# Optimization experiments

Hardware: AMD Instinct MI355X
Metric: run time of the kernel (lower is better)

Reference implementation:

```python
import jax, jax.numpy as jnp
import numpy as np

T, B, C, H, W = 4, 8, 256, 16, 16
HEADS = 8
N = H * W
TN = T * N
DH = C // HEADS
DECAY = 0.25

# STE quantizer: fwd round(clamp(x,0,1)); bwd passes grad only where 0<=x<=1
@jax.custom_vjp
def quant1(x):
    return jnp.round(jnp.clip(x, 0.0, 1.0))

def _q_fwd(x):
    return quant1(x), x

def _q_bwd(x, g):
    return (jnp.where((x < 0) | (x > 1), 0.0, g),)

quant1.defvjp(_q_fwd, _q_bwd)

def lif(x):
    # x: [T, ...]; sequential LIF membrane decay + quantize over leading (time) axis
    def step(carry, xt):
        mem_old, spike = carry
        mem = (mem_old - jax.lax.stop_gradient(spike) * 0.5) * DECAY + xt
        s = quant1(mem)
        return (mem, s), s
    z = jnp.zeros_like(x[0])
    _, out = jax.lax.scan(step, (z, z), x)
    return out

def bn1d(x, gamma, beta, mean, var):
    # eval-mode BatchNorm1d over channel axis 1 of [B, Ch, L]
    inv = jax.lax.rsqrt(var + 1e-5)
    return (x - mean[None, :, None]) * (gamma * inv)[None, :, None] + beta[None, :, None]

def _rel_pos_index():
    coords = np.stack(np.meshgrid(np.arange(T), np.arange(H), np.arange(W), indexing='ij'))  # [3,T,H,W]
    cf = coords.reshape(3, -1)                      # [3, TN]
    rc = (cf[:, :, None] - cf[:, None, :]).transpose(1, 2, 0).copy()  # [TN, TN, 3]
    rc[:, :, 0] += T - 1
    rc[:, :, 1] += H - 1
    rc[:, :, 2] += W - 1
    rc[:, :, 0] *= (2 * H - 1) * (2 * W - 1)
    rc[:, :, 1] *= (2 * W - 1)
    return rc.sum(-1)                               # [TN, TN] ints

def _mask():
    m = np.ones((TN, TN), np.float32)
    for t in range(T - 1):
        m[t * N:(t + 1) * N, (t + 1) * N:] = 0.0
    return m

_RPI = jnp.asarray(_rel_pos_index().reshape(-1))
_MASK = jnp.asarray(_mask())


def setup_inputs() -> dict:
    key = jax.random.key(0)
    ks = jax.random.split(key, 13)
    bias_rows = (2 * T - 1) * (2 * H - 1) * (2 * W - 1)
    return {
        'x': jax.random.normal(ks[0], (T, B, C, H, W), jnp.float32),
        'w_qkv': jax.random.normal(ks[1], (3 * C, C), jnp.float32) * 0.05,
        'qkv_gamma': jax.random.uniform(ks[2], (3 * C,), jnp.float32, 0.5, 1.5),
        'qkv_beta': jax.random.normal(ks[3], (3 * C,), jnp.float32) * 0.1,
        'qkv_mean': jax.random.normal(ks[4], (3 * C,), jnp.float32) * 0.1,
        'qkv_var': jax.random.uniform(ks[5], (3 * C,), jnp.float32, 0.5, 1.5),
        'bias_table': jax.random.normal(ks[6], (bias_rows, HEADS), jnp.float32) * 0.02,
        'w_proj': jax.random.normal(ks[7], (C, C), jnp.float32) * 0.05,
        'b_proj': jax.random.normal(ks[8], (C,), jnp.float32) * 0.02,
        'proj_gamma': jax.random.uniform(ks[9], (C,), jnp.float32, 0.5, 1.5),
        'proj_beta': jax.random.normal(ks[10], (C,), jnp.float32) * 0.1,
        'proj_mean': jax.random.normal(ks[11], (C,), jnp.float32) * 0.1,
        'proj_var': jax.random.uniform(ks[12], (C,), jnp.float32, 0.5, 1.5),
    }


def reference(x, w_qkv, qkv_gamma, qkv_beta, qkv_mean, qkv_var, bias_table,
              w_proj, b_proj, proj_gamma, proj_beta, proj_mean, proj_var):
    # flatten spatial, then raw reshape [T,B,C,N] -> [B,C,T*N] (as in torch source)
    xf = x.reshape(T, B, C, N).reshape(B, C, T * N)
    # 1x1 conv == channel matmul, then eval BN
    qkv = jnp.einsum('oc,bcl->bol', w_qkv, xf)
    qkv = bn1d(qkv, qkv_gamma, qkv_beta, qkv_mean, qkv_var)
    qkv = qkv.reshape(B, 3 * C, T, N).transpose(2, 0, 1, 3)  # [T,B,3C,N]
    qkv = lif(qkv).transpose(1, 0, 3, 2)                      # [B,T,N,3C]
    q, k, v = jnp.split(qkv, 3, axis=-1)                      # each [B,T,N,C]

    def to_heads(z):  # b t n (h d) -> b h (t n) d
        return z.reshape(B, T, N, HEADS, DH).transpose(0, 3, 1, 2, 4).reshape(B, HEADS, TN, DH)
    q, k, v = map(to_heads, (q, k, v))

    bias = bias_table[_RPI].reshape(TN, TN, HEADS).transpose(2, 0, 1)  # [h,TN,TN]
    attn = jnp.einsum('bhnd,bhmd->bhnm', q, k) + bias[None]
    attn = attn * _MASK[None, None]                                     # block upper-triangle mask
    o = jnp.einsum('bhnm,bhmd->bhnd', attn, v) * 0.125                  # [B,h,TN,d]

    o = o.transpose(0, 2, 1, 3).reshape(B, TN, C).reshape(B, T, N, C).transpose(1, 0, 3, 2)  # [T,B,C,N]
    o = lif(o)
    o = o.transpose(1, 2, 0, 3).reshape(B, C, T * N)          # [B,C,TN]
    o = jnp.einsum('oc,bcl->bol', w_proj, o) + b_proj[None, :, None]
    o = bn1d(o, proj_gamma, proj_beta, proj_mean, proj_var)
    o = o.reshape(B, C, T, N).transpose(2, 0, 1, 3).reshape(T, B, C, H, W)
    return lif(o)
```

## Files before the change

### kernel.cpp

```cpp
#include <hip/hip_runtime.h>
#include <stdint.h>
#include <math.h>

constexpr int T_ = 4;
constexpr int B_ = 8;
constexpr int C_ = 256;
constexpr int N_ = 256;
constexpr int TN_ = 1024;
constexpr int NH_ = 8;
constexpr int O3_ = 768;
constexpr int BIAS_ROWS_ = 6727;

__device__ __constant__ int TI_OF[10] = {0,1,1,2,2,2,3,3,3,3};
__device__ __constant__ int TJ_OF[10] = {0,0,1,0,1,2,0,1,2,3};

__device__ __forceinline__ float quant1f(float m) {
    return rintf(fminf(fmaxf(m, 0.0f), 1.0f));
}

__global__ __launch_bounds__(256) void k1_qkv_gemm(
    const float* __restrict__ x, const float* __restrict__ w,
    const float* __restrict__ gamma, const float* __restrict__ beta,
    const float* __restrict__ mean, const float* __restrict__ var,
    float* __restrict__ out)
{
    __shared__ float At[32][68];
    __shared__ float Bt[32][132];
    const int b = blockIdx.z;
    const int oBase = blockIdx.y * 64;
    const int lBase = blockIdx.x * 128;
    const int tid = threadIdx.x;
    const int tx = tid & 31;
    const int ty = tid >> 5;
    const float* xb = x + (size_t)b * C_ * TN_;

    float acc[8][4];
#pragma unroll
    for (int i = 0; i < 8; ++i)
#pragma unroll
        for (int j = 0; j < 4; ++j) acc[i][j] = 0.0f;

    const int a_row0 = tid >> 4, a_k2 = (tid & 15) * 2;
    const int b_kk0 = tid >> 5, b_c4 = (tid & 31) * 4;

    for (int kc = 0; kc < 8; ++kc) {
        const int k0 = kc * 32;
#pragma unroll
        for (int r = 0; r < 4; ++r) {
            const int row = a_row0 + 16 * r;
            const float2 v = *(const float2*)&w[(size_t)(oBase + row) * C_ + k0 + a_k2];
            At[a_k2][row] = v.x;
            At[a_k2 + 1][row] = v.y;
        }
#pragma unroll
        for (int r = 0; r < 4; ++r) {
            const int kk = b_kk0 + 8 * r;
            const float4 v = *(const float4*)&xb[(size_t)(k0 + kk) * TN_ + lBase + b_c4];
            *(float4*)&Bt[kk][b_c4] = v;
        }
        __syncthreads();
#pragma unroll
        for (int cc = 0; cc < 32; ++cc) {
            float a[8], bb[4];
            *(float4*)&a[0] = *(const float4*)&At[cc][ty * 4];
            *(float4*)&a[4] = *(const float4*)&At[cc][32 + ty * 4];
            *(float4*)&bb[0] = *(const float4*)&Bt[cc][tx * 4];
#pragma unroll
            for (int i = 0; i < 8; ++i)
#pragma unroll
                for (int j = 0; j < 4; ++j) acc[i][j] += a[i] * bb[j];
        }
        __syncthreads();
    }

#pragma unroll
    for (int i = 0; i < 8; ++i) {
        const int o = oBase + (i >> 2) * 32 + ty * 4 + (i & 3);
        const float inv = 1.0f / sqrtf(var[o] + 1e-5f);
        const float g = gamma[o] * inv;
        const float mn = mean[o], bt = beta[o];
        float4 st;
        st.x = (acc[i][0] - mn) * g + bt;
        st.y = (acc[i][1] - mn) * g + bt;
        st.z = (acc[i][2] - mn) * g + bt;
        st.w = (acc[i][3] - mn) * g + bt;
        *(float4*)&out[((size_t)b * O3_ + o) * TN_ + lBase + tx * 4] = st;
    }
}

__global__ __launch_bounds__(256) void k2_lif_pack(
    const float* __restrict__ qkv,
    uint32_t* __restrict__ qb, uint32_t* __restrict__ kb, uint32_t* __restrict__ vb)
{
    const int n = threadIdx.x;
    const int g = blockIdx.x;
    const int b = blockIdx.y;
    const int dh = blockIdx.z;
    const int which = g >> 3, h = g & 7;
    uint32_t* dstw = (which == 0) ? qb : (which == 1) ? kb : vb;
    uint16_t* dst = (uint16_t*)dstw;
    const float* src = qkv + ((size_t)b * O3_ + g * 32 + dh * 16) * TN_;

    float memv[16];
#pragma unroll
    for (int d = 0; d < 16; ++d) memv[d] = 0.0f;
    uint32_t prev = 0;

    for (int t = 0; t < T_; ++t) {
        uint32_t bits = 0;
#pragma unroll
        for (int d = 0; d < 16; ++d) {
            const float xv = src[(size_t)d * TN_ + t * N_ + n];
            const float m = (memv[d] - 0.5f * (float)((prev >> d) & 1u)) * 0.25f + xv;
            memv[d] = m;
            const float s = quant1f(m);
            bits |= ((uint32_t)s) << d;
        }
        prev = bits;
        dst[2 * (((size_t)b * NH_ + h) * TN_ + t * N_ + n) + dh] = (uint16_t)bits;
    }
}

__global__ __launch_bounds__(256) void k3_tg(
    const uint32_t* __restrict__ kb, const uint32_t* __restrict__ vb,
    float* __restrict__ Gf)
{
    __shared__ uint64_t ks[4][32][4];
    __shared__ uint64_t vs[4][32][4];
    const int bh = blockIdx.x;
    const int tid = threadIdx.x;
    const int q = tid >> 6, lane = tid & 63;

#pragma unroll
    for (int t = 0; t < T_; ++t) {
        const int j = t * N_ + q * 64 + lane;
        const uint32_t kw = kb[(size_t)bh * TN_ + j];
        const uint32_t vw = vb[(size_t)bh * TN_ + j];
#pragma unroll
        for (int d = 0; d < 32; ++d) {
            const uint64_t mk = __ballot((kw >> d) & 1u);
            const uint64_t mv = __ballot((vw >> d) & 1u);
            if (lane == 0) { ks[t][d][q] = mk; vs[t][d][q] = mv; }
        }
    }
    __syncthreads();

    const int d = tid & 31;
#pragma unroll
    for (int s = 0; s < 4; ++s) {
        const int d2 = (tid >> 5) + 8 * s;
        int cum = 0;
#pragma unroll
        for (int t = 0; t < T_; ++t) {
            int p = 0;
#pragma unroll
            for (int w = 0; w < 4; ++w) p += __popcll(ks[t][d2][w] & vs[t][d][w]);
            cum += p;
            Gf[(size_t)(bh * 4 + t) * 1024 + d2 * 32 + d] = (float)cum;
        }
    }
}

__global__ __launch_bounds__(256) void k3_bias_gemm(
    const uint32_t* __restrict__ vb, const float* __restrict__ bias_table,
    float* __restrict__ p0, float* __restrict__ p1,
    float* __restrict__ p2, float* __restrict__ p3)
{
    __shared__ float sbl[640];
    __shared__ float At[32][68];
    __shared__ float Bt[32][132];

    const int z = blockIdx.z;
    const int h = z / 10;
    const int p = z % 10;
    const int ti = TI_OF[p], tj = TJ_OF[p];
    const int dt = ti - tj;
    const int iT = blockIdx.y;
    const int nBase = blockIdx.x * 128;
    const int tid = threadIdx.x;

    const int base = 3363 + 961 * dt + 124 * iT - 480;
    for (int s = tid; s < 640; s += 256) {
        const int gidx = base + s;
        sbl[s] = (gidx < BIAS_ROWS_) ? bias_table[(size_t)gidx * NH_ + h] : 0.0f;
    }

    const int ty = tid >> 4, tx = tid & 15;

    const int iBase4 = ty * 4;
    const int sIdxBase = 31 * (iBase4 >> 4) + (iBase4 & 15) + 480 - tx;

    const int n8 = tx * 8;
    const int nS = nBase + n8;
    const int bS = nS >> 5, d0S = nS & 31;
    const uint32_t* vbw = vb + ((size_t)bS * NH_ + h) * TN_ + tj * 256 + ty;

    const int nA = nBase + tx * 4;
    const int nB = nBase + 64 + tx * 4;
    const int bA = nA >> 5, dA = nA & 31;
    const int bB = nB >> 5, dB = nB & 31;

    float acc[4][8];
#pragma unroll
    for (int i = 0; i < 4; ++i)
#pragma unroll
        for (int j = 0; j < 8; ++j) acc[i][j] = 0.0f;

    __syncthreads();

    for (int kc = 0; kc < 8; ++kc) {
#pragma unroll
        for (int r = 0; r < 2; ++r) {
            const int s0 = sIdxBase - 31 * (kc * 2 + r);
            float4 av;
            av.x = sbl[s0];
            av.y = sbl[s0 + 1];
            av.z = sbl[s0 + 2];
            av.w = sbl[s0 + 3];
            *(float4*)&At[tx + 16 * r][iBase4] = av;
        }
#pragma unroll
        for (int r = 0; r < 2; ++r) {
            const uint32_t wd = vbw[kc * 32 + 16 * r];
            float4 b0, b1;
            b0.x = (float)((wd >> d0S) & 1u);
            b0.y = (float)((wd >> (d0S + 1)) & 1u);
            b0.z = (float)((wd >> (d0S + 2)) & 1u);
            b0.w = (float)((wd >> (d0S + 3)) & 1u);
            b1.x = (float)((wd >> (d0S + 4)) & 1u);
            b1.y = (float)((wd >> (d0S + 5)) & 1u);
            b1.z = (float)((wd >> (d0S + 6)) & 1u);
            b1.w = (float)((wd >> (d0S + 7)) & 1u);
            *(float4*)&Bt[ty + 16 * r][n8] = b0;
            *(float4*)&Bt[ty + 16 * r][n8 + 4] = b1;
        }
        __syncthreads();
#pragma unroll
        for (int cc = 0; cc < 32; ++cc) {
            float a[4], bb[8];
            *(float4*)&a[0] = *(const float4*)&At[cc][ty * 4];
            *(float4*)&bb[0] = *(const float4*)&Bt[cc][tx * 4];
            *(float4*)&bb[4] = *(const float4*)&Bt[cc][64 + tx * 4];
#pragma unroll
            for (int i = 0; i < 4; ++i)
#pragma unroll
                for (int j = 0; j < 8; ++j) acc[i][j] += a[i] * bb[j];
        }
        __syncthreads();
    }

    float* plane = (tj == 0) ? p0 : (tj == 1) ? p1 : (tj == 2) ? p2 : p3;
    const int nrows = (4 - tj) * 256;
    const int cA = h * 32 + dA;
    const int cB = h * 32 + dB;
#pragma unroll
    for (int r = 0; r < 4; ++r) {
        const int rowL = dt * 256 + iT * 64 + ty * 4 + r;
        float4 s0, s1;
        s0.x = acc[r][0]; s0.y = acc[r][1]; s0.z = acc[r][2]; s0.w = acc[r][3];
        s1.x = acc[r][4]; s1.y = acc[r][5]; s1.z = acc[r][6]; s1.w = acc[r][7];
        *(float4*)&plane[((size_t)bA * nrows + rowL) * 256 + cA] = s0;
        *(float4*)&plane[((size_t)bB * nrows + rowL) * 256 + cB] = s1;
    }
}

__global__ __launch_bounds__(256) void k4_lif2(
    const uint32_t* __restrict__ qb, const float* __restrict__ Gf,
    const float* __restrict__ p0, const float* __restrict__ p1,
    const float* __restrict__ p2, const float* __restrict__ p3,
    uint32_t* __restrict__ s2c)
{
    const int c = threadIdx.x;
    const int n = blockIdx.x;
    const int b = blockIdx.y;
    const int lane = c & 63;
    const int h = c >> 5, d = c & 31;
    const int bh = b * NH_ + h;
    const uint32_t* qbh = qb + (size_t)bh * TN_;

    float memv = 0.0f, spk = 0.0f;
    for (int t = 0; t < T_; ++t) {
        const int l = t * N_ + n;
        const uint32_t q = qbh[l];
        const float* g = Gf + (size_t)(bh * 4 + t) * 1024 + d;
        float v = 0.0f;
#pragma unroll
        for (int d2 = 0; d2 < 32; ++d2)
            v += ((q >> d2) & 1u) ? g[d2 * 32] : 0.0f;
        v += p0[((size_t)b * 1024 + l) * 256 + c];
        if (t >= 1) v += p1[((size_t)b * 768 + (l - 256)) * 256 + c];
        if (t >= 2) v += p2[((size_t)b * 512 + (l - 512)) * 256 + c];
        if (t >= 3) v += p3[((size_t)b * 256 + (l - 768)) * 256 + c];
        const float m = (memv - 0.5f * spk) * 0.25f + 0.125f * v;
        memv = m;
        const float s = quant1f(m);
        spk = s;
        const uint64_t mask = __ballot(s != 0.0f);
        if (lane == 0)
            s2c[((size_t)b * TN_ + l) * 8 + (c >> 5)] = (uint32_t)mask;
        else if (lane == 32)
            s2c[((size_t)b * TN_ + l) * 8 + (c >> 5)] = (uint32_t)(mask >> 32);
    }
}

__global__ __launch_bounds__(256) void k5_proj_lif(
    const uint32_t* __restrict__ s2c, const float* __restrict__ w,
    const float* __restrict__ bp,
    const float* __restrict__ gamma, const float* __restrict__ beta,
    const float* __restrict__ mean, const float* __restrict__ var,
    float* __restrict__ out)
{
    __shared__ float At[128][36];
    __shared__ uint32_t Sw[128 * 9];
    const int nBase = blockIdx.x * 32;
    const int oBase = blockIdx.y * 32;
    const int b = blockIdx.z;
    const int tid = threadIdx.x;
    const int tx = tid & 31;
    const int ty = tid >> 5;

#pragma unroll
    for (int j = 0; j < 4; ++j) {
        const int fidx = tid * 4 + j;
        const int lp = fidx >> 3, wsel = fidx & 7;
        const int t = lp >> 5, nn = lp & 31;
        Sw[lp * 9 + wsel] = s2c[((size_t)b * TN_ + t * 256 + nBase + nn) * 8 + wsel];
    }

    const int a_row = tid >> 3, a_kq = (tid & 7) * 16;

    float acc[4][4];
#pragma unroll
    for (int r = 0; r < 4; ++r)
#pragma unroll
        for (int t = 0; t < 4; ++t) acc[r][t] = 0.0f;

    for (int half = 0; half < 2; ++half) {
        if (half) __syncthreads();
#pragma unroll
        for (int j = 0; j < 4; ++j) {
            const float4 v = *(const float4*)&w[(size_t)(oBase + a_row) * C_ + half * 128 + a_kq + 4 * j];
            At[a_kq + 4 * j][a_row] = v.x;
            At[a_kq + 4 * j + 1][a_row] = v.y;
            At[a_kq + 4 * j + 2][a_row] = v.z;
            At[a_kq + 4 * j + 3][a_row] = v.w;
        }
        __syncthreads();

        for (int ks = 0; ks < 4; ++ks) {
            uint32_t wr[4];
#pragma unroll
            for (int t = 0; t < 4; ++t)
                wr[t] = Sw[(t * 32 + tx) * 9 + half * 4 + ks];
#pragma unroll
            for (int u = 0; u < 32; ++u) {
                float a[4];
                *(float4*)&a[0] = *(const float4*)&At[ks * 32 + u][ty * 4];
                float bv[4];
#pragma unroll
                for (int t = 0; t < 4; ++t) bv[t] = (float)((wr[t] >> u) & 1u);
#pragma unroll
                for (int r = 0; r < 4; ++r)
#pragma unroll
                    for (int t = 0; t < 4; ++t) acc[r][t] += a[r] * bv[t];
            }
        }
    }

#pragma unroll
    for (int r = 0; r < 4; ++r) {
        const int o = oBase + ty * 4 + r;
        const float inv = 1.0f / sqrtf(var[o] + 1e-5f);
        const float g = gamma[o] * inv;
        const float mn = mean[o], bt = beta[o], bpo = bp[o];
        float memv = 0.0f, spk = 0.0f;
#pragma unroll
        for (int t = 0; t < 4; ++t) {
            const float val = ((acc[r][t] + bpo) - mn) * g + bt;
            const float m = (memv - 0.5f * spk) * 0.25f + val;
            memv = m;
            const float s = quant1f(m);
            spk = s;
            out[(((size_t)t * B_ + b) * C_ + o) * N_ + nBase + tx] = s;
        }
    }
}

extern "C" void kernel_launch(void* const* d_in, const int* in_sizes, int n_in,
                              void* d_out, int out_size, void* d_ws, size_t ws_size,
                              hipStream_t stream)
{
    const float* x          = (const float*)d_in[0];
    const float* w_qkv      = (const float*)d_in[1];
    const float* qkv_gamma  = (const float*)d_in[2];
    const float* qkv_beta   = (const float*)d_in[3];
    const float* qkv_mean   = (const float*)d_in[4];
    const float* qkv_var    = (const float*)d_in[5];
    const float* bias_table = (const float*)d_in[6];
    const float* w_proj     = (const float*)d_in[7];
    const float* b_proj     = (const float*)d_in[8];
    const float* proj_gamma = (const float*)d_in[9];
    const float* proj_beta  = (const float*)d_in[10];
    const float* proj_mean  = (const float*)d_in[11];
    const float* proj_var   = (const float*)d_in[12];
    float* out = (float*)d_out;

    char* ws = (char*)d_ws;
    float*    qkv_bn = (float*)(ws + 0);
    float*    part0  = (float*)(ws + 1048576);
    float*    part1  = (float*)(ws + 9437184);
    float*    part2  = (float*)(ws + 15728640);
    float*    part3  = (float*)(ws + 19922944);
    float*    Gf     = (float*)(ws + 25165824);
    uint32_t* s2c    = (uint32_t*)(ws + 33554432);
    uint32_t* qbits  = (uint32_t*)(ws + 50331648);
    uint32_t* kbits  = (uint32_t*)(ws + 50593792);
    uint32_t* vbits  = (uint32_t*)(ws + 50855936);

    k1_qkv_gemm<<<dim3(8, 12, 8), 256, 0, stream>>>(
        x, w_qkv, qkv_gamma, qkv_beta, qkv_mean, qkv_var, qkv_bn);

    k2_lif_pack<<<dim3(24, 8, 2), 256, 0, stream>>>(qkv_bn, qbits, kbits, vbits);

    k3_tg<<<dim3(64), 256, 0, stream>>>(kbits, vbits, Gf);

    k3_bias_gemm<<<dim3(2, 4, 80), 256, 0, stream>>>(
        vbits, bias_table, part0, part1, part2, part3);

    k4_lif2<<<dim3(256, 8), 256, 0, stream>>>(
        qbits, Gf, part0, part1, part2, part3, s2c);

    k5_proj_lif<<<dim3(8, 8, 8), 256, 0, stream>>>(
        s2c, w_proj, b_proj, proj_gamma, proj_beta, proj_mean, proj_var, out);
}
```

Measured before the change: 223.2 us.

## Enlarge GEMM tiles, split LIF packing finer, parallelize K^T V popcount over time

The QKV GEMM and the bias GEMM now compute 128x128 tiles with an 8x8 per-thread micro-tile instead of 64x128 tiles, which raises arithmetic intensity and cuts the number of blocks. The LIF pack kernel writes byte-sized groups of 8 channels so the grid gets twice as many blocks. The K^T V popcount kernel is split into a per-timestep kernel with four times as many blocks plus a separate cumulative-sum kernel, giving more parallelism at the cost of an extra launch and an intermediate buffer. The larger tiles use more registers and fewer blocks, which may lower occupancy.

```diff
diff --git a/kernel.cpp b/kernel.cpp
--- a/kernel.cpp
+++ b/kernel.cpp
@@ -24,21 +24,21 @@
     const float* __restrict__ mean, const float* __restrict__ var,
     float* __restrict__ out)
 {
-    __shared__ float At[32][68];
+    __shared__ float At[32][132];
     __shared__ float Bt[32][132];
-    const int b = blockIdx.z;
-    const int oBase = blockIdx.y * 64;
-    const int lBase = blockIdx.x * 128;
+    const int lTile = blockIdx.x;
+    const int oBase = blockIdx.y * 128;
+    const int b = lTile >> 3;
+    const int lBase = (lTile & 7) * 128;
     const int tid = threadIdx.x;
-    const int tx = tid & 31;
-    const int ty = tid >> 5;
+    const int ty = tid >> 4, tx = tid & 15;
     const float* xb = x + (size_t)b * C_ * TN_;
 
-    float acc[8][4];
+    float acc[8][8];
 #pragma unroll
     for (int i = 0; i < 8; ++i)
 #pragma unroll
-        for (int j = 0; j < 4; ++j) acc[i][j] = 0.0f;
+        for (int j = 0; j < 8; ++j) acc[i][j] = 0.0f;
 
     const int a_row0 = tid >> 4, a_k2 = (tid & 15) * 2;
     const int b_kk0 = tid >> 5, b_c4 = (tid & 31) * 4;
@@ -46,7 +46,7 @@
     for (int kc = 0; kc < 8; ++kc) {
         const int k0 = kc * 32;
 #pragma unroll
-        for (int r = 0; r < 4; ++r) {
+        for (int r = 0; r < 8; ++r) {
             const int row = a_row0 + 16 * r;
             const float2 v = *(const float2*)&w[(size_t)(oBase + row) * C_ + k0 + a_k2];
             At[a_k2][row] = v.x;
@@ -61,30 +61,37 @@
         __syncthreads();
 #pragma unroll
         for (int cc = 0; cc < 32; ++cc) {
-            float a[8], bb[4];
+            float a[8], bb[8];
             *(float4*)&a[0] = *(const float4*)&At[cc][ty * 4];
-            *(float4*)&a[4] = *(const float4*)&At[cc][32 + ty * 4];
+            *(float4*)&a[4] = *(const float4*)&At[cc][64 + ty * 4];
             *(float4*)&bb[0] = *(const float4*)&Bt[cc][tx * 4];
+            *(float4*)&bb[4] = *(const float4*)&Bt[cc][64 + tx * 4];
 #pragma unroll
             for (int i = 0; i < 8; ++i)
 #pragma unroll
-                for (int j = 0; j < 4; ++j) acc[i][j] += a[i] * bb[j];
+                for (int j = 0; j < 8; ++j) acc[i][j] += a[i] * bb[j];
         }
         __syncthreads();
     }
 
 #pragma unroll
     for (int i = 0; i < 8; ++i) {
-        const int o = oBase + (i >> 2) * 32 + ty * 4 + (i & 3);
+        const int o = oBase + (i >> 2) * 64 + ty * 4 + (i & 3);
         const float inv = 1.0f / sqrtf(var[o] + 1e-5f);
         const float g = gamma[o] * inv;
         const float mn = mean[o], bt = beta[o];
-        float4 st;
-        st.x = (acc[i][0] - mn) * g + bt;
-        st.y = (acc[i][1] - mn) * g + bt;
-        st.z = (acc[i][2] - mn) * g + bt;
-        st.w = (acc[i][3] - mn) * g + bt;
-        *(float4*)&out[((size_t)b * O3_ + o) * TN_ + lBase + tx * 4] = st;
+        float4 s0, s1;
+        s0.x = (acc[i][0] - mn) * g + bt;
+        s0.y = (acc[i][1] - mn) * g + bt;
+        s0.z = (acc[i][2] - mn) * g + bt;
+        s0.w = (acc[i][3] - mn) * g + bt;
+        s1.x = (acc[i][4] - mn) * g + bt;
+        s1.y = (acc[i][5] - mn) * g + bt;
+        s1.z = (acc[i][6] - mn) * g + bt;
+        s1.w = (acc[i][7] - mn) * g + bt;
+        float* dst = &out[((size_t)b * O3_ + o) * TN_ + lBase];
+        *(float4*)&dst[tx * 4] = s0;
+        *(float4*)&dst[64 + tx * 4] = s1;
     }
 }
 
@@ -95,21 +102,21 @@
     const int n = threadIdx.x;
     const int g = blockIdx.x;
     const int b = blockIdx.y;
-    const int dh = blockIdx.z;
+    const int dq = blockIdx.z;
     const int which = g >> 3, h = g & 7;
     uint32_t* dstw = (which == 0) ? qb : (which == 1) ? kb : vb;
-    uint16_t* dst = (uint16_t*)dstw;
-    const float* src = qkv + ((size_t)b * O3_ + g * 32 + dh * 16) * TN_;
-
-    float memv[16];
-#pragma unroll
-    for (int d = 0; d < 16; ++d) memv[d] = 0.0f;
+    uint8_t* dst = (uint8_t*)dstw;
+    const float* src = qkv + ((size_t)b * O3_ + g * 32 + dq * 8) * TN_;
+
+    float memv[8];
+#pragma unroll
+    for (int d = 0; d < 8; ++d) memv[d] = 0.0f;
     uint32_t prev = 0;
 
     for (int t = 0; t < T_; ++t) {
         uint32_t bits = 0;
 #pragma unroll
-        for (int d = 0; d < 16; ++d) {
+        for (int d = 0; d < 8; ++d) {
             const float xv = src[(size_t)d * TN_ + t * N_ + n];
             const float m = (memv[d] - 0.5f * (float)((prev >> d) & 1u)) * 0.25f + xv;
             memv[d] = m;
@@ -117,46 +124,56 @@
             bits |= ((uint32_t)s) << d;
         }
         prev = bits;
-        dst[2 * (((size_t)b * NH_ + h) * TN_ + t * N_ + n) + dh] = (uint16_t)bits;
-    }
-}
-
-__global__ __launch_bounds__(256) void k3_tg(
+        dst[4 * (((size_t)b * NH_ + h) * TN_ + t * N_ + n) + dq] = (uint8_t)bits;
+    }
+}
+
+__global__ __launch_bounds__(256) void k3_tgp(
     const uint32_t* __restrict__ kb, const uint32_t* __restrict__ vb,
-    float* __restrict__ Gf)
-{
-    __shared__ uint64_t ks[4][32][4];
-    __shared__ uint64_t vs[4][32][4];
+    int* __restrict__ Pt)
+{
+    __shared__ uint64_t ks[32][4];
+    __shared__ uint64_t vs[32][4];
+    const int t = blockIdx.x;
+    const int bh = blockIdx.y;
+    const int tid = threadIdx.x;
+    const int q = tid >> 6, lane = tid & 63;
+    const int j = t * N_ + q * 64 + lane;
+
+    const uint32_t kw = kb[(size_t)bh * TN_ + j];
+    const uint32_t vw = vb[(size_t)bh * TN_ + j];
+#pragma unroll
+    for (int d = 0; d < 32; ++d) {
+        const uint64_t mk = __ballot((kw >> d) & 1u);
+        const uint64_t mv = __ballot((vw >> d) & 1u);
+        if (lane == 0) { ks[d][q] = mk; vs[d][q] = mv; }
+    }
+    __syncthreads();
+
+    const int d = tid & 31;
+#pragma unroll
+    for (int s = 0; s < 4; ++s) {
+        const int d2 = (tid >> 5) + 8 * s;
+        int p = 0;
+#pragma unroll
+        for (int w = 0; w < 4; ++w) p += __popcll(ks[d2][w] & vs[d][w]);
+        Pt[(size_t)(bh * 4 + t) * 1024 + d2 * 32 + d] = p;
+    }
+}
+
+__global__ __launch_bounds__(256) void k3_cum(
+    const int* __restrict__ Pt, float* __restrict__ Gf)
+{
     const int bh = blockIdx.x;
     const int tid = threadIdx.x;
-    const int q = tid >> 6, lane = tid & 63;
-
-#pragma unroll
-    for (int t = 0; t < T_; ++t) {
-        const int j = t * N_ + q * 64 + lane;
-        const uint32_t kw = kb[(size_t)bh * TN_ + j];
-        const uint32_t vw = vb[(size_t)bh * TN_ + j];
-#pragma unroll
-        for (int d = 0; d < 32; ++d) {
-            const uint64_t mk = __ballot((kw >> d) & 1u);
-            const uint64_t mv = __ballot((vw >> d) & 1u);
-            if (lane == 0) { ks[t][d][q] = mk; vs[t][d][q] = mv; }
-        }
-    }
-    __syncthreads();
-
-    const int d = tid & 31;
-#pragma unroll
-    for (int s = 0; s < 4; ++s) {
-        const int d2 = (tid >> 5) + 8 * s;
+#pragma unroll
+    for (int r = 0; r < 4; ++r) {
+        const int idx = tid + 256 * r;
         int cum = 0;
 #pragma unroll
         for (int t = 0; t < T_; ++t) {
-            int p = 0;
-#pragma unroll
-            for (int w = 0; w < 4; ++w) p += __popcll(ks[t][d2][w] & vs[t][d][w]);
-            cum += p;
-            Gf[(size_t)(bh * 4 + t) * 1024 + d2 * 32 + d] = (float)cum;
+            cum += Pt[(size_t)(bh * 4 + t) * 1024 + idx];
+            Gf[(size_t)(bh * 4 + t) * 1024 + idx] = (float)cum;
         }
     }
 }
@@ -166,8 +183,8 @@
     float* __restrict__ p0, float* __restrict__ p1,
     float* __restrict__ p2, float* __restrict__ p3)
 {
-    __shared__ float sbl[640];
-    __shared__ float At[32][68];
+    __shared__ float sbl[720];
+    __shared__ float At[32][132];
     __shared__ float Bt[32][132];
 
     const int z = blockIdx.z;
@@ -179,16 +196,20 @@
     const int nBase = blockIdx.x * 128;
     const int tid = threadIdx.x;
 
-    const int base = 3363 + 961 * dt + 124 * iT - 480;
-    for (int s = tid; s < 640; s += 256) {
+    const int base = 3363 + 961 * dt + 248 * iT - 480;
+    for (int s = tid; s < 720; s += 256) {
         const int gidx = base + s;
-        sbl[s] = (gidx < BIAS_ROWS_) ? bias_table[(size_t)gidx * NH_ + h] : 0.0f;
+        sbl[s] = (gidx >= 0 && gidx < BIAS_ROWS_) ? bias_table[(size_t)gidx * NH_ + h] : 0.0f;
     }
 
     const int ty = tid >> 4, tx = tid & 15;
 
-    const int iBase4 = ty * 4;
-    const int sIdxBase = 31 * (iBase4 >> 4) + (iBase4 & 15) + 480 - tx;
+    int sRow[2];
+#pragma unroll
+    for (int g = 0; g < 2; ++g) {
+        const int il = g * 64 + ty * 4;
+        sRow[g] = 31 * (il >> 4) + (il & 15) + 480 - tx;
+    }
 
     const int n8 = tx * 8;
     const int nS = nBase + n8;
@@ -200,9 +221,9 @@
     const int bA = nA >> 5, dA = nA & 31;
     const int bB = nB >> 5, dB = nB & 31;
 
-    float acc[4][8];
-#pragma unroll
-    for (int i = 0; i < 4; ++i)
+    float acc[8][8];
+#pragma unroll
+    for (int i = 0; i < 8; ++i)
 #pragma unroll
         for (int j = 0; j < 8; ++j) acc[i][j] = 0.0f;
 
@@ -210,14 +231,18 @@
 
     for (int kc = 0; kc < 8; ++kc) {
 #pragma unroll
-        for (int r = 0; r < 2; ++r) {
-            const int s0 = sIdxBase - 31 * (kc * 2 + r);
-            float4 av;
-            av.x = sbl[s0];
-            av.y = sbl[s0 + 1];
-            av.z = sbl[s0 + 2];
-            av.w = sbl[s0 + 3];
-            *(float4*)&At[tx + 16 * r][iBase4] = av;
+        for (int r1 = 0; r1 < 2; ++r1) {
+            const int shift = 31 * (kc * 2 + r1);
+#pragma unroll
+            for (int g = 0; g < 2; ++g) {
+                const int s0 = sRow[g] - shift;
+                float4 av;
+                av.x = sbl[s0];
+                av.y = sbl[s0 + 1];
+                av.z = sbl[s0 + 2];
+                av.w = sbl[s0 + 3];
+                *(float4*)&At[tx + 16 * r1][g * 64 + ty * 4] = av;
+            }
         }
 #pragma unroll
         for (int r = 0; r < 2; ++r) {
@@ -237,12 +262,13 @@
         __syncthreads();
 #pragma unroll
         for (int cc = 0; cc < 32; ++cc) {
-            float a[4], bb[8];
+            float a[8], bb[8];
             *(float4*)&a[0] = *(const float4*)&At[cc][ty * 4];
+            *(float4*)&a[4] = *(const float4*)&At[cc][64 + ty * 4];
             *(float4*)&bb[0] = *(const float4*)&Bt[cc][tx * 4];
             *(float4*)&bb[4] = *(const float4*)&Bt[cc][64 + tx * 4];
 #pragma unroll
-            for (int i = 0; i < 4; ++i)
+            for (int i = 0; i < 8; ++i)
 #pragma unroll
                 for (int j = 0; j < 8; ++j) acc[i][j] += a[i] * bb[j];
         }
@@ -254,11 +280,11 @@
     const int cA = h * 32 + dA;
     const int cB = h * 32 + dB;
 #pragma unroll
-    for (int r = 0; r < 4; ++r) {
-        const int rowL = dt * 256 + iT * 64 + ty * 4 + r;
+    for (int i = 0; i < 8; ++i) {
+        const int rowL = dt * 256 + iT * 128 + (i >> 2) * 64 + ty * 4 + (i & 3);
         float4 s0, s1;
-        s0.x = acc[r][0]; s0.y = acc[r][1]; s0.z = acc[r][2]; s0.w = acc[r][3];
-        s1.x = acc[r][4]; s1.y = acc[r][5]; s1.z = acc[r][6]; s1.w = acc[r][7];
+        s0.x = acc[i][0]; s0.y = acc[i][1]; s0.z = acc[i][2]; s0.w = acc[i][3];
+        s1.x = acc[i][4]; s1.y = acc[i][5]; s1.z = acc[i][6]; s1.w = acc[i][7];
         *(float4*)&plane[((size_t)bA * nrows + rowL) * 256 + cA] = s0;
         *(float4*)&plane[((size_t)bB * nrows + rowL) * 256 + cB] = s1;
     }
@@ -412,19 +438,22 @@
     float*    part2  = (float*)(ws + 15728640);
     float*    part3  = (float*)(ws + 19922944);
     float*    Gf     = (float*)(ws + 25165824);
+    int*      Pt     = (int*)  (ws + 26214400);
     uint32_t* s2c    = (uint32_t*)(ws + 33554432);
     uint32_t* qbits  = (uint32_t*)(ws + 50331648);
     uint32_t* kbits  = (uint32_t*)(ws + 50593792);
     uint32_t* vbits  = (uint32_t*)(ws + 50855936);
 
-    k1_qkv_gemm<<<dim3(8, 12, 8), 256, 0, stream>>>(
+    k1_qkv_gemm<<<dim3(64, 6), 256, 0, stream>>>(
         x, w_qkv, qkv_gamma, qkv_beta, qkv_mean, qkv_var, qkv_bn);
 
-    k2_lif_pack<<<dim3(24, 8, 2), 256, 0, stream>>>(qkv_bn, qbits, kbits, vbits);
-
-    k3_tg<<<dim3(64), 256, 0, stream>>>(kbits, vbits, Gf);
-
-    k3_bias_gemm<<<dim3(2, 4, 80), 256, 0, stream>>>(
+    k2_lif_pack<<<dim3(24, 8, 4), 256, 0, stream>>>(qkv_bn, qbits, kbits, vbits);
+
+    k3_tgp<<<dim3(4, 64), 256, 0, stream>>>(kbits, vbits, Pt);
+
+    k3_cum<<<dim3(64), 256, 0, stream>>>(Pt, Gf);
+
+    k3_bias_gemm<<<dim3(2, 2, 80), 256, 0, stream>>>(
         vbits, bias_table, part0, part1, part2, part3);
 
     k4_lif2<<<dim3(256, 8), 256, 0, stream>>>(
```

Measured after the change: 229.3 us. 1.03x slower.
